# Kernel optimization log

Measured on AMD Instinct MI355X. Metric: run time of the kernel, lower is better.

The kernel has to match this reference:

```python
import jax, jax.numpy as jnp
import numpy as np

B, N, DIM, H = 8, 1024, 1024, 8
HEAD_DIM = DIM // H
SCALE = HEAD_DIM ** -0.5  # scale_with_head=True


def setup_inputs() -> dict:
    key = jax.random.key(0)
    k1, k2, k3, k4 = jax.random.split(key, 4)
    return {
        "q": jax.random.normal(k1, (B, N, DIM), dtype=jnp.float32),
        "k": jax.random.normal(k2, (B, N, DIM), dtype=jnp.float32),
        "v": jax.random.normal(k3, (B, N, DIM), dtype=jnp.float32),
        "W_out": jax.random.normal(k4, (DIM, DIM), dtype=jnp.float32) * (DIM ** -0.5),
        "b_out": jnp.zeros((DIM,), dtype=jnp.float32),
    }


def reference(q, k, v, W_out, b_out):
    b, n, dim = q.shape
    h, d = H, dim // H
    # b n (h d) -> b h n d
    def split_heads(t):
        return t.reshape(b, n, h, d).transpose(0, 2, 1, 3)
    qh, kh, vh = split_heads(q), split_heads(k), split_heads(v)
    dots = jnp.einsum('bhid,bhjd->bhij', qh, kh) * SCALE
    attn = jax.nn.softmax(dots, axis=-1)
    out = jnp.einsum('bhij,bhjd->bhid', attn, vh)
    out = out.transpose(0, 2, 1, 3).reshape(b, n, dim)  # b h n d -> b n (h d)
    out = out @ W_out.T + b_out  # nn.Linear(dim, dim); dropout p=0 is identity
    return out, attn
```

## Files before the change

### kernel.cpp

```cpp
#include <hip/hip_runtime.h>

typedef __bf16 bf16x8 __attribute__((ext_vector_type(8)));
typedef unsigned short u16x8 __attribute__((ext_vector_type(8)));
typedef unsigned short u16x4 __attribute__((ext_vector_type(4)));
typedef float f32x4 __attribute__((ext_vector_type(4)));

#define B_    8
#define N_    1024
#define DIM_  1024
#define H_    8
#define HD_   128
#define SCALE_ 0.08838834764831845f

__device__ __forceinline__ unsigned short f2bf(float x) {
  unsigned int u = __float_as_uint(x);
  u += 0x7fffu + ((u >> 16) & 1u);
  return (unsigned short)(u >> 16);
}
__device__ __forceinline__ float bf2f(unsigned short h) {
  return __uint_as_float(((unsigned int)h) << 16);
}
__device__ __forceinline__ f32x4 mfma16(u16x8 a, u16x8 b, f32x4 c) {
  return __builtin_amdgcn_mfma_f32_16x16x32_bf16(
      __builtin_bit_cast(bf16x8, a), __builtin_bit_cast(bf16x8, b), c, 0, 0, 0);
}
__device__ __forceinline__ void gl_lds16(const void* g, void* l) {
  __builtin_amdgcn_global_load_lds(
      (const __attribute__((address_space(1))) unsigned int*)g,
      (__attribute__((address_space(3))) unsigned int*)l, 16, 0, 0);
}
#define SBAR() do { asm volatile("" ::: "memory"); __builtin_amdgcn_s_barrier(); \
                    asm volatile("" ::: "memory"); } while (0)
#define LGKM0() do { asm volatile("s_waitcnt lgkmcnt(0)" ::: "memory"); \
                     __builtin_amdgcn_sched_barrier(0); } while (0)

#define WS_KIMG  0
#define WS_VIMG  33554432
#define WS_WHI   67108864
#define WS_WLO   69206016
#define WS_AOHI  71303168
#define WS_AOLO  88080384

__global__ __launch_bounds__(256)
void prep_k(const float* __restrict__ gk, char* __restrict__ kimg) {
  const int blk = blockIdx.x;
  const int bh = blk >> 4, it = blk & 15;
  const int bb = bh >> 3, hh = bh & 7;
  const int t = threadIdx.x;
  char* base = kimg + (size_t)bh * 524288 + it * 32768;
  const float* src = gk + ((size_t)bb * N_ + it * 64) * DIM_ + hh * HD_;
  #pragma unroll
  for (int c = 0; c < 8; ++c) {
    const int idx = t + 256 * c;
    const int key = idx >> 5, dq = (idx & 31) * 4;
    f32x4 f = *(const f32x4*)(src + (size_t)key * DIM_ + dq);
    u16x4 h, g;
    #pragma unroll
    for (int j = 0; j < 4; ++j) {
      unsigned short hv = f2bf(f[j]);
      h[j] = hv;
      g[j] = f2bf(f[j] - bf2f(hv));
    }
    const int dh = dq >> 6, dloc = dq & 63;
    const int off = (dloc * 2) ^ ((key & 7) << 4);
    char* dst = base + dh * 16384 + key * 256;
    *(u16x4*)(dst + off) = h;
    *(u16x4*)(dst + 128 + off) = g;
  }
}

__global__ __launch_bounds__(256)
void prep_v(const float* __restrict__ gv, char* __restrict__ vimg) {
  __shared__ float tile[32][132];
  const int blk = blockIdx.x;
  const int bh = blk >> 5, kt = blk & 31;
  const int bb = bh >> 3, hh = bh & 7;
  const int t = threadIdx.x;
  const float* src = gv + ((size_t)bb * N_ + kt * 32) * DIM_ + hh * HD_;
  #pragma unroll
  for (int c = 0; c < 4; ++c) {
    const int idx = t + 256 * c;
    const int key = idx >> 5, dq = (idx & 31) * 4;
    *(f32x4*)&tile[key][dq] = *(const f32x4*)(src + (size_t)key * DIM_ + dq);
  }
  __syncthreads();
  char* base = vimg + (size_t)bh * 524288 + kt * 16384;
  #pragma unroll
  for (int c = 0; c < 2; ++c) {
    const int oc = t + 256 * c;
    const int d = oc >> 2, kc = oc & 3;
    u16x8 h, g;
    #pragma unroll
    for (int j = 0; j < 8; ++j) {
      float x = tile[kc * 8 + j][d];
      unsigned short hv = f2bf(x);
      h[j] = hv;
      g[j] = f2bf(x - bf2f(hv));
    }
    const int off = (d * 64 + kc * 16) ^ ((d & 7) << 4);
    *(u16x8*)(base + off) = h;
    *(u16x8*)(base + 8192 + off) = g;
  }
}

__global__ __launch_bounds__(256)
void prep_w(const float* __restrict__ gw, unsigned short* __restrict__ whi,
            unsigned short* __restrict__ wlo) {
  const int idx = blockIdx.x * 256 + threadIdx.x;
  const int row = idx >> 7, k0 = (idx & 127) * 8;
  const float* s = gw + (size_t)row * DIM_ + k0;
  f32x4 f0 = *(const f32x4*)s;
  f32x4 f1 = *(const f32x4*)(s + 4);
  u16x8 h, g;
  #pragma unroll
  for (int j = 0; j < 8; ++j) {
    float x = j < 4 ? f0[j] : f1[j - 4];
    unsigned short hv = f2bf(x);
    h[j] = hv;
    g[j] = f2bf(x - bf2f(hv));
  }
  *(u16x8*)(whi + (size_t)row * DIM_ + k0) = h;
  *(u16x8*)(wlo + (size_t)row * DIM_ + k0) = g;
}

struct K1Smem {
  unsigned short p[64 * 1024];
  union {
    char kb[2][16384];
    char vt[2][16384];
    struct { char pad[16384]; float partial[4][64]; float rinv[64]; } pp;
  } u;
};

__global__ __launch_bounds__(512, 2)
void attn_kernel(const float* __restrict__ gq, const char* __restrict__ kimg,
                 const char* __restrict__ vimg, float* __restrict__ gattn,
                 unsigned short* __restrict__ aohi, unsigned short* __restrict__ aolo) {
  __shared__ K1Smem sm;
  const int bid = blockIdx.x;
  const int xcd = bid & 7, slot = bid >> 3;
  const int bh = xcd + 8 * (slot >> 4);
  const int qt = slot & 15;
  const int bb = bh >> 3, hh = bh & 7;

  const int tid = threadIdx.x;
  const int wid = tid >> 6, lane = tid & 63;
  const int rg = wid >> 2;
  const int kg = wid & 3;
  const int l15 = lane & 15, l4 = lane >> 4;

  const char* kimg_bh = kimg + (size_t)bh * 524288;
  const char* vimg_bh = vimg + (size_t)bh * 524288;

  auto issueK = [&](int s) {
    const char* src = kimg_bh + s * 16384 + wid * 2048 + lane * 16;
    char* dst = sm.u.kb[s & 1] + wid * 2048;
    gl_lds16(src, dst);
    gl_lds16(src + 1024, dst + 1024);
  };
  auto issueV = [&](int kt) {
    const char* src = vimg_bh + kt * 16384 + wid * 2048 + lane * 16;
    char* dst = sm.u.vt[kt & 1] + wid * 2048;
    gl_lds16(src, dst);
    gl_lds16(src + 1024, dst + 1024);
  };

  issueK(0);

  u16x8 qhi[2][4], qlo[2][4];
  #pragma unroll
  for (int rt = 0; rt < 2; ++rt) {
    const int qrow = qt * 64 + rg * 32 + rt * 16 + l15;
    const float* qp = gq + ((size_t)bb * N_ + qrow) * DIM_ + hh * HD_;
    #pragma unroll
    for (int t = 0; t < 4; ++t) {
      const int d0 = t * 32 + l4 * 8;
      f32x4 f0 = *(const f32x4*)(qp + d0);
      f32x4 f1 = *(const f32x4*)(qp + d0 + 4);
      #pragma unroll
      for (int j = 0; j < 8; ++j) {
        float x = (j < 4 ? f0[j] : f1[j - 4]) * SCALE_;
        unsigned short hi = f2bf(x);
        qhi[rt][t][j] = hi;
        qlo[rt][t][j] = f2bf(x - bf2f(hi));
      }
    }
  }

  issueK(1);
  asm volatile("s_waitcnt vmcnt(2)" ::: "memory");
  SBAR();

  float lsum0 = 0.f, lsum1 = 0.f;
  const int key16 = kg * 16 + l15;
  const int kswz = (key16 & 7) << 4;
  const char* krow0 = sm.u.kb[0] + key16 * 256;
  const char* krow1 = sm.u.kb[1] + key16 * 256;
  char* const prow0 = (char*)sm.p + (rg * 32 + l15) * 2048;
  char* const prow1 = (char*)sm.p + (rg * 32 + 16 + l15) * 2048;
  const int pswz0 = ((rg * 32 + l15) & 7) << 4;
  const int pswz1 = ((rg * 32 + 16 + l15) & 7) << 4;

  f32x4 a0[2], a1[2], a2[2];
  #pragma unroll 2
  for (int s = 0; s < 32; ++s) {
    const int dh = s & 1;
    if (s >= 1 && s < 31) issueK(s + 1);
    else if (s == 31) issueV(0);
    const char* krow = dh ? krow1 : krow0;
    u16x8 khi[2], klo[2];
    #pragma unroll
    for (int tl = 0; tl < 2; ++tl) {
      const int off = (tl * 64 + l4 * 16) ^ kswz;
      khi[tl] = *(const u16x8*)(krow + off);
      klo[tl] = *(const u16x8*)(krow + 128 + off);
    }
    if (dh == 0) {
      #pragma unroll
      for (int rt = 0; rt < 2; ++rt) {
        a0[rt] = f32x4{0.f, 0.f, 0.f, 0.f};
        a1[rt] = f32x4{0.f, 0.f, 0.f, 0.f};
        a2[rt] = f32x4{0.f, 0.f, 0.f, 0.f};
      }
    }
    #pragma unroll
    for (int tl = 0; tl < 2; ++tl) {
      const int t = dh * 2 + tl;
      #pragma unroll
      for (int rt = 0; rt < 2; ++rt) {
        a0[rt] = mfma16(khi[tl], qhi[rt][t], a0[rt]);
        a1[rt] = mfma16(klo[tl], qhi[rt][t], a1[rt]);
        a2[rt] = mfma16(khi[tl], qlo[rt][t], a2[rt]);
      }
    }
    if (dh == 1) {
      const int keyb = ((s >> 1) * 64 + kg * 16 + l4 * 4) * 2;
      #pragma unroll
      for (int rt = 0; rt < 2; ++rt) {
        u16x4 pk;
        float ls = 0.f;
        #pragma unroll
        for (int r = 0; r < 4; ++r) {
          float sv = (a0[rt][r] + a1[rt][r]) + a2[rt][r];
          sv = fminf(sv, 60.0f);
          float p = __expf(sv);
          ls += p;
          pk[r] = f2bf(p);
        }
        if (rt == 0) { lsum0 += ls; *(u16x4*)(prow0 + (keyb ^ pswz0)) = pk; }
        else         { lsum1 += ls; *(u16x4*)(prow1 + (keyb ^ pswz1)) = pk; }
      }
    }
    if (s < 31) { asm volatile("s_waitcnt vmcnt(0)" ::: "memory"); }
    else        { asm volatile("s_waitcnt vmcnt(2)" ::: "memory"); }
    SBAR();
  }

  {
    float s0 = lsum0; s0 += __shfl_xor(s0, 16); s0 += __shfl_xor(s0, 32);
    float s1 = lsum1; s1 += __shfl_xor(s1, 16); s1 += __shfl_xor(s1, 32);
    if (lane < 16) {
      sm.u.pp.partial[kg][rg * 32 + lane] = s0;
      sm.u.pp.partial[kg][rg * 32 + 16 + lane] = s1;
    }
  }
  LGKM0();
  SBAR();
  if (tid < 64) {
    float t4 = sm.u.pp.partial[0][tid] + sm.u.pp.partial[1][tid] +
               sm.u.pp.partial[2][tid] + sm.u.pp.partial[3][tid];
    sm.u.pp.rinv[tid] = 1.0f / t4;
  }
  LGKM0();
  SBAR();
  float rvf[2][4];
  #pragma unroll
  for (int rt = 0; rt < 2; ++rt)
    #pragma unroll
    for (int r = 0; r < 4; ++r)
      rvf[rt][r] = sm.u.pp.rinv[rg * 32 + rt * 16 + l4 * 4 + r];
  const bool writer = (kg < 2);
  float rvw = 0.f;
  if (writer) rvw = sm.u.pp.rinv[rg * 32 + kg * 16 + l15];
  LGKM0();
  asm volatile("s_waitcnt vmcnt(0)" ::: "memory");
  SBAR();

  f32x4 oacc[2][2];
  #pragma unroll
  for (int rt = 0; rt < 2; ++rt)
    #pragma unroll
    for (int ct = 0; ct < 2; ++ct) oacc[rt][ct] = f32x4{0.f, 0.f, 0.f, 0.f};

  float* arow = nullptr;
  if (writer)
    arow = gattn + ((size_t)bh * N_ + qt * 64 + rg * 32 + kg * 16 + l15) * N_ + l4 * 8;

  #pragma unroll 2
  for (int kt = 0; kt < 32; ++kt) {
    if (kt < 31) issueV(kt + 1);
    const char* vbase = sm.u.vt[kt & 1];
    u16x8 vh[2], vl[2];
    #pragma unroll
    for (int ct = 0; ct < 2; ++ct) {
      const int d = kg * 32 + ct * 16 + l15;
      const int off = (d * 64 + l4 * 16) ^ ((d & 7) << 4);
      vh[ct] = *(const u16x8*)(vbase + off);
      vl[ct] = *(const u16x8*)(vbase + 8192 + off);
    }
    const int pb = kt * 64 + l4 * 16;
    u16x8 pa0 = *(const u16x8*)(prow0 + (pb ^ pswz0));
    u16x8 pa1 = *(const u16x8*)(prow1 + (pb ^ pswz1));
    #pragma unroll
    for (int ct = 0; ct < 2; ++ct) {
      oacc[0][ct] = mfma16(pa0, vh[ct], oacc[0][ct]);
      oacc[0][ct] = mfma16(pa0, vl[ct], oacc[0][ct]);
      oacc[1][ct] = mfma16(pa1, vh[ct], oacc[1][ct]);
      oacc[1][ct] = mfma16(pa1, vl[ct], oacc[1][ct]);
    }
    if (writer) {
      u16x8 pw = (kg == 0) ? pa0 : pa1;
      f32x4 o0, o1;
      o0[0] = bf2f(pw[0]) * rvw; o0[1] = bf2f(pw[1]) * rvw;
      o0[2] = bf2f(pw[2]) * rvw; o0[3] = bf2f(pw[3]) * rvw;
      o1[0] = bf2f(pw[4]) * rvw; o1[1] = bf2f(pw[5]) * rvw;
      o1[2] = bf2f(pw[6]) * rvw; o1[3] = bf2f(pw[7]) * rvw;
      __builtin_nontemporal_store(o0, (f32x4*)(arow + kt * 32));
      __builtin_nontemporal_store(o1, (f32x4*)(arow + kt * 32 + 4));
    }
    if (kt < 31) {
      if (writer) asm volatile("s_waitcnt vmcnt(2)" ::: "memory");
      else        asm volatile("s_waitcnt vmcnt(0)" ::: "memory");
    }
    SBAR();
  }

  #pragma unroll
  for (int rt = 0; rt < 2; ++rt)
    #pragma unroll
    for (int ct = 0; ct < 2; ++ct) {
      const int col = hh * HD_ + kg * 32 + ct * 16 + l15;
      const int row0 = bb * N_ + qt * 64 + rg * 32 + rt * 16 + l4 * 4;
      #pragma unroll
      for (int r = 0; r < 4; ++r) {
        float val = oacc[rt][ct][r] * rvf[rt][r];
        unsigned short hv = f2bf(val);
        unsigned short lv = f2bf(val - bf2f(hv));
        const size_t off = (size_t)(row0 + r) * DIM_ + col;
        __builtin_nontemporal_store(hv, aohi + off);
        __builtin_nontemporal_store(lv, aolo + off);
      }
    }
}

struct K2Smem {
  unsigned short A[128 * 2 * 32];
  unsigned short Bm[128 * 2 * 32];
};

__global__ __launch_bounds__(512)
void proj_kernel(const unsigned short* __restrict__ aohi, const unsigned short* __restrict__ aolo,
                 const unsigned short* __restrict__ whi, const unsigned short* __restrict__ wlo,
                 const float* __restrict__ gbias, float* __restrict__ gout) {
  __shared__ K2Smem sm;
  const int bid = blockIdx.x;
  const int mt = bid >> 3, nt = bid & 7;
  const int m0 = mt * 128, n0 = nt * 128;
  const int tid = threadIdx.x;
  const int wid = tid >> 6, lane = tid & 63;
  const int wr = wid >> 1, wc = wid & 1;
  const int l15 = lane & 15, l4 = lane >> 4;

  f32x4 acc[2][4];
  #pragma unroll
  for (int i = 0; i < 2; ++i)
    #pragma unroll
    for (int j = 0; j < 4; ++j) acc[i][j] = f32x4{0.f, 0.f, 0.f, 0.f};

  #pragma unroll 1
  for (int step = 0; step < 32; ++step) {
    const int k0 = step * 32;
    if (step) __syncthreads();
    #pragma unroll
    for (int c0 = 0; c0 < 4; ++c0) {
      const int c = tid + 512 * c0;
      const int mat = c >> 10;
      const int cc = c & 1023;
      const int row = cc >> 3, hl = (cc >> 2) & 1, ch = cc & 3;
      const unsigned short* plane = mat == 0 ? (hl ? aolo : aohi) : (hl ? wlo : whi);
      const size_t grow = (size_t)((mat == 0 ? m0 : n0) + row);
      u16x8 vdat = *(const u16x8*)(plane + grow * DIM_ + k0 + ch * 8);
      char* lbase = (mat == 0 ? (char*)sm.A : (char*)sm.Bm) + row * 128;
      *(u16x8*)(lbase + ((hl * 64 + ch * 16) ^ ((row & 7) << 4))) = vdat;
    }
    __syncthreads();

    u16x8 ah[2], al[2], bh[4], bl[4];
    #pragma unroll
    for (int t = 0; t < 2; ++t) {
      const int row = wr * 32 + t * 16 + l15;
      const char* rp = (char*)sm.A + row * 128;
      const int swz = (row & 7) << 4;
      ah[t] = *(const u16x8*)(rp + ((l4 * 16) ^ swz));
      al[t] = *(const u16x8*)(rp + ((64 + l4 * 16) ^ swz));
    }
    #pragma unroll
    for (int t = 0; t < 4; ++t) {
      const int col = wc * 64 + t * 16 + l15;
      const char* rp = (char*)sm.Bm + col * 128;
      const int swz = (col & 7) << 4;
      bh[t] = *(const u16x8*)(rp + ((l4 * 16) ^ swz));
      bl[t] = *(const u16x8*)(rp + ((64 + l4 * 16) ^ swz));
    }
    #pragma unroll
    for (int i = 0; i < 2; ++i)
      #pragma unroll
      for (int j = 0; j < 4; ++j)
        acc[i][j] = mfma16(ah[i], bh[j], acc[i][j]);
    #pragma unroll
    for (int i = 0; i < 2; ++i)
      #pragma unroll
      for (int j = 0; j < 4; ++j)
        acc[i][j] = mfma16(ah[i], bl[j], acc[i][j]);
    #pragma unroll
    for (int i = 0; i < 2; ++i)
      #pragma unroll
      for (int j = 0; j < 4; ++j)
        acc[i][j] = mfma16(al[i], bh[j], acc[i][j]);
  }

  #pragma unroll
  for (int i = 0; i < 2; ++i) {
    #pragma unroll
    for (int j = 0; j < 4; ++j) {
      const int col = n0 + wc * 64 + j * 16 + l15;
      const float bv = gbias[col];
      float* dst = gout + (size_t)(m0 + wr * 32 + i * 16 + l4 * 4) * DIM_ + col;
      #pragma unroll
      for (int r = 0; r < 4; ++r)
        dst[(size_t)r * DIM_] = acc[i][j][r] + bv;
    }
  }
}

extern "C" void kernel_launch(void* const* d_in, const int* in_sizes, int n_in,
                              void* d_out, int out_size, void* d_ws, size_t ws_size,
                              hipStream_t stream) {
  const float* q    = (const float*)d_in[0];
  const float* k    = (const float*)d_in[1];
  const float* v    = (const float*)d_in[2];
  const float* W    = (const float*)d_in[3];
  const float* bias = (const float*)d_in[4];
  float* out  = (float*)d_out;
  float* attn = out + (size_t)B_ * N_ * DIM_;

  char* ws = (char*)d_ws;
  char* kimg = ws + WS_KIMG;
  char* vimg = ws + WS_VIMG;
  unsigned short* whi  = (unsigned short*)(ws + WS_WHI);
  unsigned short* wlo  = (unsigned short*)(ws + WS_WLO);
  unsigned short* aohi = (unsigned short*)(ws + WS_AOHI);
  unsigned short* aolo = (unsigned short*)(ws + WS_AOLO);

  prep_k<<<64 * 16, 256, 0, stream>>>(k, kimg);
  prep_v<<<64 * 32, 256, 0, stream>>>(v, vimg);
  prep_w<<<512, 256, 0, stream>>>(W, whi, wlo);
  attn_kernel<<<B_ * H_ * (N_ / 64), 512, 0, stream>>>(q, kimg, vimg, attn, aohi, aolo);
  proj_kernel<<<(B_ * N_ / 128) * (DIM_ / 128), 512, 0, stream>>>(aohi, aolo, whi, wlo, bias, out);
}
```

Measured before the change: 273.4 us.

## Double attention waves per block and pre-tile projection operands for async LDS loads

The attention kernel now runs 1024 threads per block, with each wave owning 16 query rows instead of 32. This halves per-wave register and MFMA work and aims to raise occupancy, with s_setprio added around the MFMA sections. The attention output and W are written as pre-swizzled tile images, so the projection kernel can use double-buffered global_load_lds with 64x64 tiles and an XCD-aware block mapping. The trade-off is smaller per-wave tiles with less operand reuse, more blocks, and more barrier overhead.

```diff
diff --git a/kernel.cpp b/kernel.cpp
--- a/kernel.cpp
+++ b/kernel.cpp
@@ -33,13 +33,12 @@
                     asm volatile("" ::: "memory"); } while (0)
 #define LGKM0() do { asm volatile("s_waitcnt lgkmcnt(0)" ::: "memory"); \
                      __builtin_amdgcn_sched_barrier(0); } while (0)
-
-#define WS_KIMG  0
-#define WS_VIMG  33554432
-#define WS_WHI   67108864
-#define WS_WLO   69206016
-#define WS_AOHI  71303168
-#define WS_AOLO  88080384
+#define VMC(n)  asm volatile("s_waitcnt vmcnt(" #n ")" ::: "memory")
+
+#define WS_KIMG  ((size_t)0)
+#define WS_VIMG  ((size_t)32 << 20)
+#define WS_WIMG  ((size_t)64 << 20)
+#define WS_AOIMG ((size_t)68 << 20)
 
 __global__ __launch_bounds__(256)
 void prep_k(const float* __restrict__ gk, char* __restrict__ kimg) {
@@ -104,11 +103,10 @@
 }
 
 __global__ __launch_bounds__(256)
-void prep_w(const float* __restrict__ gw, unsigned short* __restrict__ whi,
-            unsigned short* __restrict__ wlo) {
+void prep_w(const float* __restrict__ gw, char* __restrict__ wimg) {
   const int idx = blockIdx.x * 256 + threadIdx.x;
-  const int row = idx >> 7, k0 = (idx & 127) * 8;
-  const float* s = gw + (size_t)row * DIM_ + k0;
+  const int row = idx >> 7, c0 = (idx & 127) * 8;
+  const float* s = gw + (size_t)row * DIM_ + c0;
   f32x4 f0 = *(const f32x4*)s;
   f32x4 f1 = *(const f32x4*)(s + 4);
   u16x8 h, g;
@@ -119,8 +117,12 @@
     h[j] = hv;
     g[j] = f2bf(x - bf2f(hv));
   }
-  *(u16x8*)(whi + (size_t)row * DIM_ + k0) = h;
-  *(u16x8*)(wlo + (size_t)row * DIM_ + k0) = g;
+  const int nt = row >> 6, rl = row & 63;
+  const int st = c0 >> 5, kl = c0 & 31;
+  char* base = wimg + ((size_t)(nt * 32 + st) * 64 + rl) * 128;
+  const int swz = (rl & 7) << 4;
+  *(u16x8*)(base + ((kl * 2) ^ swz)) = h;
+  *(u16x8*)(base + ((64 + kl * 2) ^ swz)) = g;
 }
 
 struct K1Smem {
@@ -132,10 +134,10 @@
   } u;
 };
 
-__global__ __launch_bounds__(512, 2)
+__global__ __launch_bounds__(1024, 4)
 void attn_kernel(const float* __restrict__ gq, const char* __restrict__ kimg,
                  const char* __restrict__ vimg, float* __restrict__ gattn,
-                 unsigned short* __restrict__ aohi, unsigned short* __restrict__ aolo) {
+                 char* __restrict__ aoimg) {
   __shared__ K1Smem sm;
   const int bid = blockIdx.x;
   const int xcd = bid & 7, slot = bid >> 3;
@@ -153,24 +155,19 @@
   const char* vimg_bh = vimg + (size_t)bh * 524288;
 
   auto issueK = [&](int s) {
-    const char* src = kimg_bh + s * 16384 + wid * 2048 + lane * 16;
-    char* dst = sm.u.kb[s & 1] + wid * 2048;
-    gl_lds16(src, dst);
-    gl_lds16(src + 1024, dst + 1024);
+    const char* src = kimg_bh + s * 16384 + wid * 1024 + lane * 16;
+    gl_lds16(src, sm.u.kb[s & 1] + wid * 1024);
   };
   auto issueV = [&](int kt) {
-    const char* src = vimg_bh + kt * 16384 + wid * 2048 + lane * 16;
-    char* dst = sm.u.vt[kt & 1] + wid * 2048;
-    gl_lds16(src, dst);
-    gl_lds16(src + 1024, dst + 1024);
+    const char* src = vimg_bh + kt * 16384 + wid * 1024 + lane * 16;
+    gl_lds16(src, sm.u.vt[kt & 1] + wid * 1024);
   };
 
   issueK(0);
 
-  u16x8 qhi[2][4], qlo[2][4];
-  #pragma unroll
-  for (int rt = 0; rt < 2; ++rt) {
-    const int qrow = qt * 64 + rg * 32 + rt * 16 + l15;
+  u16x8 qhi[4], qlo[4];
+  {
+    const int qrow = qt * 64 + rg * 16 + l15;
     const float* qp = gq + ((size_t)bb * N_ + qrow) * DIM_ + hh * HD_;
     #pragma unroll
     for (int t = 0; t < 4; ++t) {
@@ -181,27 +178,26 @@
       for (int j = 0; j < 8; ++j) {
         float x = (j < 4 ? f0[j] : f1[j - 4]) * SCALE_;
         unsigned short hi = f2bf(x);
-        qhi[rt][t][j] = hi;
-        qlo[rt][t][j] = f2bf(x - bf2f(hi));
+        qhi[t][j] = hi;
+        qlo[t][j] = f2bf(x - bf2f(hi));
       }
     }
   }
 
   issueK(1);
-  asm volatile("s_waitcnt vmcnt(2)" ::: "memory");
+  VMC(1);
   SBAR();
 
-  float lsum0 = 0.f, lsum1 = 0.f;
+  float lsum = 0.f;
   const int key16 = kg * 16 + l15;
   const int kswz = (key16 & 7) << 4;
   const char* krow0 = sm.u.kb[0] + key16 * 256;
   const char* krow1 = sm.u.kb[1] + key16 * 256;
-  char* const prow0 = (char*)sm.p + (rg * 32 + l15) * 2048;
-  char* const prow1 = (char*)sm.p + (rg * 32 + 16 + l15) * 2048;
-  const int pswz0 = ((rg * 32 + l15) & 7) << 4;
-  const int pswz1 = ((rg * 32 + 16 + l15) & 7) << 4;
-
-  f32x4 a0[2], a1[2], a2[2];
+  const int prow_i = rg * 16 + l15;
+  char* const prow = (char*)sm.p + prow_i * 2048;
+  const int pswz = (prow_i & 7) << 4;
+
+  f32x4 a0, a1, a2;
   #pragma unroll 2
   for (int s = 0; s < 32; ++s) {
     const int dh = s & 1;
@@ -216,53 +212,43 @@
       klo[tl] = *(const u16x8*)(krow + 128 + off);
     }
     if (dh == 0) {
-      #pragma unroll
-      for (int rt = 0; rt < 2; ++rt) {
-        a0[rt] = f32x4{0.f, 0.f, 0.f, 0.f};
-        a1[rt] = f32x4{0.f, 0.f, 0.f, 0.f};
-        a2[rt] = f32x4{0.f, 0.f, 0.f, 0.f};
-      }
-    }
+      a0 = f32x4{0.f, 0.f, 0.f, 0.f};
+      a1 = f32x4{0.f, 0.f, 0.f, 0.f};
+      a2 = f32x4{0.f, 0.f, 0.f, 0.f};
+    }
+    __builtin_amdgcn_s_setprio(1);
     #pragma unroll
     for (int tl = 0; tl < 2; ++tl) {
       const int t = dh * 2 + tl;
-      #pragma unroll
-      for (int rt = 0; rt < 2; ++rt) {
-        a0[rt] = mfma16(khi[tl], qhi[rt][t], a0[rt]);
-        a1[rt] = mfma16(klo[tl], qhi[rt][t], a1[rt]);
-        a2[rt] = mfma16(khi[tl], qlo[rt][t], a2[rt]);
-      }
-    }
+      a0 = mfma16(khi[tl], qhi[t], a0);
+      a1 = mfma16(klo[tl], qhi[t], a1);
+      a2 = mfma16(khi[tl], qlo[t], a2);
+    }
+    __builtin_amdgcn_s_setprio(0);
     if (dh == 1) {
       const int keyb = ((s >> 1) * 64 + kg * 16 + l4 * 4) * 2;
+      u16x4 pk;
+      float ls = 0.f;
       #pragma unroll
-      for (int rt = 0; rt < 2; ++rt) {
-        u16x4 pk;
-        float ls = 0.f;
-        #pragma unroll
-        for (int r = 0; r < 4; ++r) {
-          float sv = (a0[rt][r] + a1[rt][r]) + a2[rt][r];
-          sv = fminf(sv, 60.0f);
-          float p = __expf(sv);
-          ls += p;
-          pk[r] = f2bf(p);
-        }
-        if (rt == 0) { lsum0 += ls; *(u16x4*)(prow0 + (keyb ^ pswz0)) = pk; }
-        else         { lsum1 += ls; *(u16x4*)(prow1 + (keyb ^ pswz1)) = pk; }
+      for (int r = 0; r < 4; ++r) {
+        float sv = (a0[r] + a1[r]) + a2[r];
+        sv = fminf(sv, 60.0f);
+        float p = __expf(sv);
+        ls += p;
+        pk[r] = f2bf(p);
       }
-    }
-    if (s < 31) { asm volatile("s_waitcnt vmcnt(0)" ::: "memory"); }
-    else        { asm volatile("s_waitcnt vmcnt(2)" ::: "memory"); }
+      lsum += ls;
+      *(u16x4*)(prow + (keyb ^ pswz)) = pk;
+    }
+    if (s < 31) VMC(0);
     SBAR();
   }
 
   {
-    float s0 = lsum0; s0 += __shfl_xor(s0, 16); s0 += __shfl_xor(s0, 32);
-    float s1 = lsum1; s1 += __shfl_xor(s1, 16); s1 += __shfl_xor(s1, 32);
-    if (lane < 16) {
-      sm.u.pp.partial[kg][rg * 32 + lane] = s0;
-      sm.u.pp.partial[kg][rg * 32 + 16 + lane] = s1;
-    }
+    float s0 = lsum;
+    s0 += __shfl_xor(s0, 16);
+    s0 += __shfl_xor(s0, 32);
+    if (lane < 16) sm.u.pp.partial[kg][rg * 16 + lane] = s0;
   }
   LGKM0();
   SBAR();
@@ -273,28 +259,24 @@
   }
   LGKM0();
   SBAR();
-  float rvf[2][4];
-  #pragma unroll
-  for (int rt = 0; rt < 2; ++rt)
-    #pragma unroll
-    for (int r = 0; r < 4; ++r)
-      rvf[rt][r] = sm.u.pp.rinv[rg * 32 + rt * 16 + l4 * 4 + r];
-  const bool writer = (kg < 2);
+  float rvf[4];
+  #pragma unroll
+  for (int r = 0; r < 4; ++r)
+    rvf[r] = sm.u.pp.rinv[rg * 16 + l4 * 4 + r];
+  const bool writer = (kg == 0);
   float rvw = 0.f;
-  if (writer) rvw = sm.u.pp.rinv[rg * 32 + kg * 16 + l15];
+  if (writer) rvw = sm.u.pp.rinv[prow_i];
   LGKM0();
-  asm volatile("s_waitcnt vmcnt(0)" ::: "memory");
+  VMC(0);
   SBAR();
 
-  f32x4 oacc[2][2];
-  #pragma unroll
-  for (int rt = 0; rt < 2; ++rt)
-    #pragma unroll
-    for (int ct = 0; ct < 2; ++ct) oacc[rt][ct] = f32x4{0.f, 0.f, 0.f, 0.f};
+  f32x4 oacc[2];
+  oacc[0] = f32x4{0.f, 0.f, 0.f, 0.f};
+  oacc[1] = f32x4{0.f, 0.f, 0.f, 0.f};
 
   float* arow = nullptr;
   if (writer)
-    arow = gattn + ((size_t)bh * N_ + qt * 64 + rg * 32 + kg * 16 + l15) * N_ + l4 * 8;
+    arow = gattn + ((size_t)bh * N_ + qt * 64 + prow_i) * N_ + l4 * 8;
 
   #pragma unroll 2
   for (int kt = 0; kt < 32; ++kt) {
@@ -308,138 +290,125 @@
       vh[ct] = *(const u16x8*)(vbase + off);
       vl[ct] = *(const u16x8*)(vbase + 8192 + off);
     }
-    const int pb = kt * 64 + l4 * 16;
-    u16x8 pa0 = *(const u16x8*)(prow0 + (pb ^ pswz0));
-    u16x8 pa1 = *(const u16x8*)(prow1 + (pb ^ pswz1));
+    u16x8 pa = *(const u16x8*)(prow + ((kt * 64 + l4 * 16) ^ pswz));
+    __builtin_amdgcn_s_setprio(1);
     #pragma unroll
     for (int ct = 0; ct < 2; ++ct) {
-      oacc[0][ct] = mfma16(pa0, vh[ct], oacc[0][ct]);
-      oacc[0][ct] = mfma16(pa0, vl[ct], oacc[0][ct]);
-      oacc[1][ct] = mfma16(pa1, vh[ct], oacc[1][ct]);
-      oacc[1][ct] = mfma16(pa1, vl[ct], oacc[1][ct]);
-    }
+      oacc[ct] = mfma16(pa, vh[ct], oacc[ct]);
+      oacc[ct] = mfma16(pa, vl[ct], oacc[ct]);
+    }
+    __builtin_amdgcn_s_setprio(0);
     if (writer) {
-      u16x8 pw = (kg == 0) ? pa0 : pa1;
       f32x4 o0, o1;
-      o0[0] = bf2f(pw[0]) * rvw; o0[1] = bf2f(pw[1]) * rvw;
-      o0[2] = bf2f(pw[2]) * rvw; o0[3] = bf2f(pw[3]) * rvw;
-      o1[0] = bf2f(pw[4]) * rvw; o1[1] = bf2f(pw[5]) * rvw;
-      o1[2] = bf2f(pw[6]) * rvw; o1[3] = bf2f(pw[7]) * rvw;
+      o0[0] = bf2f(pa[0]) * rvw; o0[1] = bf2f(pa[1]) * rvw;
+      o0[2] = bf2f(pa[2]) * rvw; o0[3] = bf2f(pa[3]) * rvw;
+      o1[0] = bf2f(pa[4]) * rvw; o1[1] = bf2f(pa[5]) * rvw;
+      o1[2] = bf2f(pa[6]) * rvw; o1[3] = bf2f(pa[7]) * rvw;
       __builtin_nontemporal_store(o0, (f32x4*)(arow + kt * 32));
       __builtin_nontemporal_store(o1, (f32x4*)(arow + kt * 32 + 4));
     }
+    LGKM0();
     if (kt < 31) {
-      if (writer) asm volatile("s_waitcnt vmcnt(2)" ::: "memory");
-      else        asm volatile("s_waitcnt vmcnt(0)" ::: "memory");
+      if (writer) { VMC(2); }
+      else        { VMC(0); }
     }
     SBAR();
   }
 
-  #pragma unroll
-  for (int rt = 0; rt < 2; ++rt)
+  {
+    char* aobase = aoimg + ((size_t)((bb * 16 + qt) * 32 + hh * 4 + kg)) * 8192;
     #pragma unroll
     for (int ct = 0; ct < 2; ++ct) {
-      const int col = hh * HD_ + kg * 32 + ct * 16 + l15;
-      const int row0 = bb * N_ + qt * 64 + rg * 32 + rt * 16 + l4 * 4;
+      const int colloc = ct * 16 + l15;
       #pragma unroll
       for (int r = 0; r < 4; ++r) {
-        float val = oacc[rt][ct][r] * rvf[rt][r];
+        const int rl = rg * 16 + l4 * 4 + r;
+        const int swz = (rl & 7) << 4;
+        float val = oacc[ct][r] * rvf[r];
         unsigned short hv = f2bf(val);
         unsigned short lv = f2bf(val - bf2f(hv));
-        const size_t off = (size_t)(row0 + r) * DIM_ + col;
-        __builtin_nontemporal_store(hv, aohi + off);
-        __builtin_nontemporal_store(lv, aolo + off);
+        char* rp = aobase + rl * 128;
+        __builtin_nontemporal_store(hv, (unsigned short*)(rp + ((colloc * 2) ^ swz)));
+        __builtin_nontemporal_store(lv, (unsigned short*)(rp + ((64 + colloc * 2) ^ swz)));
       }
     }
+  }
 }
 
 struct K2Smem {
-  unsigned short A[128 * 2 * 32];
-  unsigned short Bm[128 * 2 * 32];
+  char A[2][8192];
+  char Bm[2][8192];
 };
 
 __global__ __launch_bounds__(512)
-void proj_kernel(const unsigned short* __restrict__ aohi, const unsigned short* __restrict__ aolo,
-                 const unsigned short* __restrict__ whi, const unsigned short* __restrict__ wlo,
+void proj_kernel(const char* __restrict__ aoimg, const char* __restrict__ wimg,
                  const float* __restrict__ gbias, float* __restrict__ gout) {
   __shared__ K2Smem sm;
-  const int bid = blockIdx.x;
-  const int mt = bid >> 3, nt = bid & 7;
-  const int m0 = mt * 128, n0 = nt * 128;
+  const int orig = blockIdx.x;
+  const int xcd = orig & 7, idx = orig >> 3;
+  const int nt = xcd * 2 + (idx >> 7);
+  const int mt = idx & 127;
   const int tid = threadIdx.x;
   const int wid = tid >> 6, lane = tid & 63;
-  const int wr = wid >> 1, wc = wid & 1;
+  const int wr = wid >> 2, wc = wid & 3;
   const int l15 = lane & 15, l4 = lane >> 4;
 
-  f32x4 acc[2][4];
-  #pragma unroll
-  for (int i = 0; i < 2; ++i)
-    #pragma unroll
-    for (int j = 0; j < 4; ++j) acc[i][j] = f32x4{0.f, 0.f, 0.f, 0.f};
-
-  #pragma unroll 1
-  for (int step = 0; step < 32; ++step) {
-    const int k0 = step * 32;
-    if (step) __syncthreads();
-    #pragma unroll
-    for (int c0 = 0; c0 < 4; ++c0) {
-      const int c = tid + 512 * c0;
-      const int mat = c >> 10;
-      const int cc = c & 1023;
-      const int row = cc >> 3, hl = (cc >> 2) & 1, ch = cc & 3;
-      const unsigned short* plane = mat == 0 ? (hl ? aolo : aohi) : (hl ? wlo : whi);
-      const size_t grow = (size_t)((mat == 0 ? m0 : n0) + row);
-      u16x8 vdat = *(const u16x8*)(plane + grow * DIM_ + k0 + ch * 8);
-      char* lbase = (mat == 0 ? (char*)sm.A : (char*)sm.Bm) + row * 128;
-      *(u16x8*)(lbase + ((hl * 64 + ch * 16) ^ ((row & 7) << 4))) = vdat;
-    }
-    __syncthreads();
-
-    u16x8 ah[2], al[2], bh[4], bl[4];
+  auto issue = [&](int s) {
+    const char* sa = aoimg + ((size_t)(mt * 32 + s)) * 8192 + wid * 1024 + lane * 16;
+    gl_lds16(sa, sm.A[s & 1] + wid * 1024);
+    const char* sb = wimg + ((size_t)(nt * 32 + s)) * 8192 + wid * 1024 + lane * 16;
+    gl_lds16(sb, sm.Bm[s & 1] + wid * 1024);
+  };
+
+  f32x4 acc[2];
+  acc[0] = f32x4{0.f, 0.f, 0.f, 0.f};
+  acc[1] = f32x4{0.f, 0.f, 0.f, 0.f};
+
+  issue(0);
+  VMC(0);
+  SBAR();
+  #pragma unroll 2
+  for (int s = 0; s < 32; ++s) {
+    if (s < 31) issue(s + 1);
+    const char* Ab = sm.A[s & 1];
+    const char* Bb = sm.Bm[s & 1];
+    u16x8 ah[2], al[2], bh, bl;
     #pragma unroll
     for (int t = 0; t < 2; ++t) {
       const int row = wr * 32 + t * 16 + l15;
-      const char* rp = (char*)sm.A + row * 128;
+      const char* rp = Ab + row * 128;
       const int swz = (row & 7) << 4;
       ah[t] = *(const u16x8*)(rp + ((l4 * 16) ^ swz));
       al[t] = *(const u16x8*)(rp + ((64 + l4 * 16) ^ swz));
     }
-    #pragma unroll
-    for (int t = 0; t < 4; ++t) {
-      const int col = wc * 64 + t * 16 + l15;
-      const char* rp = (char*)sm.Bm + col * 128;
+    {
+      const int col = wc * 16 + l15;
+      const char* rp = Bb + col * 128;
       const int swz = (col & 7) << 4;
-      bh[t] = *(const u16x8*)(rp + ((l4 * 16) ^ swz));
-      bl[t] = *(const u16x8*)(rp + ((64 + l4 * 16) ^ swz));
-    }
-    #pragma unroll
-    for (int i = 0; i < 2; ++i)
-      #pragma unroll
-      for (int j = 0; j < 4; ++j)
-        acc[i][j] = mfma16(ah[i], bh[j], acc[i][j]);
-    #pragma unroll
-    for (int i = 0; i < 2; ++i)
-      #pragma unroll
-      for (int j = 0; j < 4; ++j)
-        acc[i][j] = mfma16(ah[i], bl[j], acc[i][j]);
-    #pragma unroll
-    for (int i = 0; i < 2; ++i)
-      #pragma unroll
-      for (int j = 0; j < 4; ++j)
-        acc[i][j] = mfma16(al[i], bh[j], acc[i][j]);
-  }
-
+      bh = *(const u16x8*)(rp + ((l4 * 16) ^ swz));
+      bl = *(const u16x8*)(rp + ((64 + l4 * 16) ^ swz));
+    }
+    __builtin_amdgcn_s_setprio(1);
+    #pragma unroll
+    for (int i = 0; i < 2; ++i) {
+      acc[i] = mfma16(ah[i], bh, acc[i]);
+      acc[i] = mfma16(ah[i], bl, acc[i]);
+      acc[i] = mfma16(al[i], bh, acc[i]);
+    }
+    __builtin_amdgcn_s_setprio(0);
+    LGKM0();
+    if (s < 31) VMC(0);
+    SBAR();
+  }
+
+  const int col = nt * 64 + wc * 16 + l15;
+  const float bv = gbias[col];
   #pragma unroll
   for (int i = 0; i < 2; ++i) {
-    #pragma unroll
-    for (int j = 0; j < 4; ++j) {
-      const int col = n0 + wc * 64 + j * 16 + l15;
-      const float bv = gbias[col];
-      float* dst = gout + (size_t)(m0 + wr * 32 + i * 16 + l4 * 4) * DIM_ + col;
-      #pragma unroll
-      for (int r = 0; r < 4; ++r)
-        dst[(size_t)r * DIM_] = acc[i][j][r] + bv;
-    }
+    float* dst = gout + (size_t)(mt * 64 + wr * 32 + i * 16 + l4 * 4) * DIM_ + col;
+    #pragma unroll
+    for (int r = 0; r < 4; ++r)
+      dst[(size_t)r * DIM_] = acc[i][r] + bv;
   }
 }
 
@@ -455,16 +424,14 @@
   float* attn = out + (size_t)B_ * N_ * DIM_;
 
   char* ws = (char*)d_ws;
-  char* kimg = ws + WS_KIMG;
-  char* vimg = ws + WS_VIMG;
-  unsigned short* whi  = (unsigned short*)(ws + WS_WHI);
-  unsigned short* wlo  = (unsigned short*)(ws + WS_WLO);
-  unsigned short* aohi = (unsigned short*)(ws + WS_AOHI);
-  unsigned short* aolo = (unsigned short*)(ws + WS_AOLO);
+  char* kimg  = ws + WS_KIMG;
+  char* vimg  = ws + WS_VIMG;
+  char* wimg  = ws + WS_WIMG;
+  char* aoimg = ws + WS_AOIMG;
 
   prep_k<<<64 * 16, 256, 0, stream>>>(k, kimg);
   prep_v<<<64 * 32, 256, 0, stream>>>(v, vimg);
-  prep_w<<<512, 256, 0, stream>>>(W, whi, wlo);
-  attn_kernel<<<B_ * H_ * (N_ / 64), 512, 0, stream>>>(q, kimg, vimg, attn, aohi, aolo);
-  proj_kernel<<<(B_ * N_ / 128) * (DIM_ / 128), 512, 0, stream>>>(aohi, aolo, whi, wlo, bias, out);
-}
+  prep_w<<<512, 256, 0, stream>>>(W, wimg);
+  attn_kernel<<<B_ * H_ * (N_ / 64), 1024, 0, stream>>>(q, kimg, vimg, attn, aoimg);
+  proj_kernel<<<2048, 512, 0, stream>>>(aoimg, wimg, bias, out);
+}
```

New measurement: 278.1 us. No clear change (+1.7%).
